# Performance work log

Hardware: AMD Instinct MI355X
Metric: run time of the kernel (lower is better)

The kernel has to match this reference:

```python
import jax, jax.numpy as jnp
import numpy as np

EPS = 1e-6
SIGMA = 0.1  # temperature for pseudo-LBS blend weights


def _quat_rotate(q, v):
    # q: [..., 4] (w, x, y, z) unit quaternions, v: [..., 3]
    qw, qv = q[..., :1], q[..., 1:]
    t = 2.0 * jnp.cross(qv, v)
    return v + qw * t + jnp.cross(qv, t)


def _pairwise_sqdist(a, b):
    # a: [n, d], b: [m, d] -> [n, m]
    return (jnp.sum(a * a, -1, keepdims=True)
            + jnp.sum(b * b, -1)[None, :]
            - 2.0 * (a @ b.T))


def setup_inputs() -> dict:
    N, K, F, V, J, P, M, H = 300000, 80, 64, 6890, 24, 64, 64, 128
    key = jax.random.key(0)
    ks = jax.random.split(key, 16)
    s = lambda i, shape: jax.random.normal(ks[i], shape, dtype=jnp.float32) * 0.05
    return {
        "xyz": jax.random.normal(ks[0], (N, 3), dtype=jnp.float32),
        "feature": jax.random.normal(ks[1], (N, F), dtype=jnp.float32),
        "centers": jax.random.normal(ks[2], (K, F), dtype=jnp.float32),
        "smpl_verts": jax.random.normal(ks[3], (V, 3), dtype=jnp.float32),
        "skinning_weights": jax.random.uniform(ks[4], (V, J), dtype=jnp.float32),
        "body_pose_feature": jax.random.normal(ks[5], (J, P), dtype=jnp.float32),
        "w_body": s(6, (P + F, M)),
        "b_body": jnp.zeros((M,), jnp.float32),
        "w_pos1": s(7, (3 + M, H)),
        "b_pos1": jnp.zeros((H,), jnp.float32),
        "w_pos2": s(8, (H, M)),
        "b_pos2": jnp.zeros((M,), jnp.float32),
        "w_rot": s(9, (M, 4)),
        "b_rot": jnp.zeros((4,), jnp.float32),
        "w_trans": s(10, (M, 3)),
        "b_trans": jnp.zeros((3,), jnp.float32),
    }


def reference(xyz, feature, centers, smpl_verts, skinning_weights,
              body_pose_feature, w_body, b_body, w_pos1, b_pos1,
              w_pos2, b_pos2, w_rot, b_rot, w_trans, b_trans):
    # ---- soft k-means: soft assignment of N points to K garment joints ----
    a = jax.nn.softmax(-_pairwise_sqdist(feature, centers), axis=-1)  # [N, K]
    cnt = a.sum(axis=0) + EPS                                          # [K]
    # weighted segment-reduce: c_assign^T @ xyz, diag(1/count) normalize
    joint_xyz = (a.T @ xyz) / cnt[:, None]      # [K, 3]
    joint_feat = (a.T @ feature) / cnt[:, None]  # [K, F] (cluster centers)

    # ---- KNN (k=1) skin-weight lookup against SMPL canonical verts ----
    idx = jnp.argmin(_pairwise_sqdist(joint_xyz, smpl_verts), axis=-1)  # [K]
    pts_W = skinning_weights[idx]                                        # [K, J]

    # ---- garment pose decoder ----
    body_feat = pts_W @ body_pose_feature                 # [K, P]
    g = jnp.concatenate([body_feat, joint_feat], axis=-1)  # [K, P+F]
    g = jax.nn.gelu(g @ w_body + b_body)                   # [K, M]
    lo, hi = smpl_verts.min(0), smpl_verts.max(0)
    xn = 2.0 * (joint_xyz - lo) / (hi - lo + EPS) - 1.0    # aabb sym-normalize
    h = jax.nn.relu(jnp.concatenate([xn, g], -1) @ w_pos1 + b_pos1)
    g2 = h @ w_pos2 + b_pos2                               # [K, M]
    q = g2 @ w_rot + b_rot
    q = q / (jnp.linalg.norm(q, axis=-1, keepdims=True) + EPS)  # [K, 4]
    t = g2 @ w_trans + b_trans                                   # [K, 3]

    # ---- pseudo-LBS: blend per-joint transforms back to N points ----
    w = jax.nn.softmax(-_pairwise_sqdist(xyz, joint_xyz) / SIGMA, axis=-1)  # [N, K]
    qb = w @ q
    qb = qb / (jnp.linalg.norm(qb, axis=-1, keepdims=True) + EPS)  # [N, 4]
    deformed_xyz = _quat_rotate(qb, xyz) + w @ t                    # [N, 3]
    return deformed_xyz
```

## Files before the change

### kernel.cpp

```cpp
#include <hip/hip_runtime.h>
#include <math.h>

#define N_PTS 300000
#define NJ 80
#define FDIM 64
#define VN 6890
#define ITER_PTS 128
#define NITER ((N_PTS + ITER_PTS - 1) / ITER_PTS)
#define GRID_A 768
#define RSLICE 16

typedef __attribute__((ext_vector_type(8))) short short8;
typedef __attribute__((ext_vector_type(4))) float f32x4;

union Frag { uint32_t u[4]; short8 v; };

__device__ __forceinline__ uint32_t pack1(float f) {
  uint32_t b = __float_as_uint(f);
  float lo = f - __uint_as_float(b & 0xFFFF0000u);
  return (b >> 16) | ((__float_as_uint(lo) >> 16) << 16);
}
__device__ __forceinline__ void unpack8(const uint32_t* W, uint32_t* hw, uint32_t* lw) {
#pragma unroll
  for (int j = 0; j < 4; ++j) {
    hw[j] = (W[2*j] & 0xFFFFu) | (W[2*j+1] << 16);
    lw[j] = (W[2*j] >> 16) | (W[2*j+1] & 0xFFFF0000u);
  }
}

__global__ __launch_bounds__(512, 6) void kA(
    const float* __restrict__ xyz, const float* __restrict__ feature,
    const float* __restrict__ centers, float* __restrict__ jacc,
    float* __restrict__ part)
{
  __shared__ uint32_t sC[NJ][68];
  __shared__ float    sCn[NJ];
  __shared__ ushort   sP[NJ][136];

  const int tid = threadIdx.x;
  const int w = tid >> 6;
  const int l = tid & 63;
  const int i = l & 15;
  const int g = l >> 4;

  for (int idx = tid; idx < NJ * 16; idx += 512) {
    int k = idx >> 4, q = idx & 15;
    float4 v = ((const float4*)centers)[k * 16 + q];
    sC[k][4*q+0] = pack1(v.x); sC[k][4*q+1] = pack1(v.y);
    sC[k][4*q+2] = pack1(v.z); sC[k][4*q+3] = pack1(v.w);
  }
  if (tid < NJ) {
    float s = 0.f;
    const float* c = centers + tid * FDIM;
    for (int d = 0; d < FDIM; ++d) s += c[d] * c[d];
    sCn[tid] = s;
  }
  __syncthreads();

  float cnv[5];
#pragma unroll
  for (int nt = 0; nt < 5; ++nt) cnv[nt] = sCn[i + 16*nt];

  f32x4 acc2[5];
#pragma unroll
  for (int nt = 0; nt < 5; ++nt) acc2[nt] = (f32x4){0.f, 0.f, 0.f, 0.f};

  for (int it = blockIdx.x; it < NITER; it += GRID_A) {
    const int base = it * ITER_PTS;

    const int ptA = base + 16*w + i;
    const int ptAc = ptA < N_PTS ? ptA : N_PTS - 1;
    const bool vA = ptA < N_PTS;
    f32x4 acc1[5];
#pragma unroll
    for (int nt = 0; nt < 5; ++nt) acc1[nt] = (f32x4){0.f, 0.f, 0.f, 0.f};

#pragma unroll
    for (int ks = 0; ks < 2; ++ks) {
      const float* fp = feature + (size_t)ptAc * FDIM + 32*ks + 8*g;
      uint32_t pw[8];
#pragma unroll
      for (int e = 0; e < 8; ++e) pw[e] = vA ? pack1(fp[e]) : 0u;
      Frag ah, al; unpack8(pw, ah.u, al.u);
#pragma unroll
      for (int nt = 0; nt < 5; ++nt) {
        uint32_t W[8];
        *(uint4*)&W[0] = *(const uint4*)&sC[i + 16*nt][32*ks + 8*g];
        *(uint4*)&W[4] = *(const uint4*)&sC[i + 16*nt][32*ks + 8*g + 4];
        Frag bh, bl; unpack8(W, bh.u, bl.u);
        acc1[nt] = __builtin_amdgcn_mfma_f32_16x16x32_bf16(ah.v, bh.v, acc1[nt], 0, 0, 0);
        acc1[nt] = __builtin_amdgcn_mfma_f32_16x16x32_bf16(ah.v, bl.v, acc1[nt], 0, 0, 0);
        acc1[nt] = __builtin_amdgcn_mfma_f32_16x16x32_bf16(al.v, bh.v, acc1[nt], 0, 0, 0);
      }
    }

#pragma unroll
    for (int r = 0; r < 4; ++r) {
      float lg[5]; float m = -1e30f;
#pragma unroll
      for (int nt = 0; nt < 5; ++nt) {
        lg[nt] = 2.f * acc1[nt][r] - cnv[nt];
        m = fmaxf(m, lg[nt]);
      }
#pragma unroll
      for (int ms = 1; ms < 16; ms <<= 1) m = fmaxf(m, __shfl_xor(m, ms));
      float ev[5], s = 0.f;
#pragma unroll
      for (int nt = 0; nt < 5; ++nt) { ev[nt] = __expf(lg[nt] - m); s += ev[nt]; }
#pragma unroll
      for (int ms = 1; ms < 16; ms <<= 1) s += __shfl_xor(s, ms);
      const float rs = 1.f / s;
      const int slot = 16*w + 4*g + r;
      const bool val = (base + slot) < N_PTS;
#pragma unroll
      for (int nt = 0; nt < 5; ++nt) {
        const int row = i + 16*nt;
        ushort h = val ? (ushort)(__float_as_uint(ev[nt] * rs) >> 16) : (ushort)0;
        sP[row][slot ^ ((row & 7) << 3)] = h;
      }
    }
    __syncthreads();

    if (w < 5) {
#pragma unroll
      for (int kk = 0; kk < 4; ++kk) {
        Frag af;
#pragma unroll
        for (int p2 = 0; p2 < 4; ++p2) {
          float x0, x1;
#pragma unroll
          for (int h = 0; h < 2; ++h) {
            const int e = 2*p2 + h;
            const int pt = base + 32*kk + 8*g + e;
            const int ptc = pt < N_PTS ? pt : N_PTS - 1;
            float x;
            if (w < 4) x = feature[(size_t)ptc * FDIM + 16*w + i];
            else       x = (i < 3) ? xyz[(size_t)ptc * 3 + i] : (i == 3 ? 1.f : 0.f);
            if (h == 0) x0 = x; else x1 = x;
          }
          af.u[p2] = (__float_as_uint(x0) >> 16) | (__float_as_uint(x1) & 0xFFFF0000u);
        }
#pragma unroll
        for (int nt = 0; nt < 5; ++nt) {
          const int row = i + 16*nt;
          const int start = (32*kk + 8*g) ^ ((row & 7) << 3);
          Frag bf;
          *(uint4*)bf.u = *(const uint4*)&sP[row][start];
          acc2[nt] = __builtin_amdgcn_mfma_f32_16x16x32_bf16(af.v, bf.v, acc2[nt], 0, 0, 0);
        }
      }
    }
    __syncthreads();
  }

  if (w < 5) {
#pragma unroll
    for (int nt = 0; nt < 5; ++nt) {
      const int joint = i + 16*nt;
#pragma unroll
      for (int r = 0; r < 4; ++r) {
        const int c = 16*w + 4*g + r;
        if (c < 68) {
          if (part) part[(size_t)blockIdx.x * 5440 + joint * 68 + c] = acc2[nt][r];
          else atomicAdd(&jacc[joint * 68 + c], acc2[nt][r]);
        }
      }
    }
  }
}

__global__ __launch_bounds__(256) void kR(const float* __restrict__ part,
                                          float* __restrict__ jacc)
{
  const int bx = blockIdx.x;
  const int cg = bx % 22, sl = bx / 22;
  const int t = cg * 256 + threadIdx.x;
  if (t >= 5440) return;
  const int b0 = sl * (GRID_A / RSLICE), b1 = b0 + GRID_A / RSLICE;
  float s0 = 0.f, s1 = 0.f, s2 = 0.f, s3 = 0.f;
  for (int b = b0; b < b1; b += 4) {
    s0 += part[(size_t)(b+0) * 5440 + t];
    s1 += part[(size_t)(b+1) * 5440 + t];
    s2 += part[(size_t)(b+2) * 5440 + t];
    s3 += part[(size_t)(b+3) * 5440 + t];
  }
  atomicAdd(&jacc[t], (s0 + s1) + (s2 + s3));
}

__global__ __launch_bounds__(64) void kB(
    const float* __restrict__ jacc, const float* __restrict__ smpl,
    const float* __restrict__ sw, const float* __restrict__ bpf,
    const float* __restrict__ w_body, const float* __restrict__ b_body,
    const float* __restrict__ w_pos1, const float* __restrict__ b_pos1,
    const float* __restrict__ w_pos2, const float* __restrict__ b_pos2,
    const float* __restrict__ w_rot,  const float* __restrict__ b_rot,
    const float* __restrict__ w_trans,const float* __restrict__ b_trans,
    float* __restrict__ jpack, float* __restrict__ qpack,
    float* __restrict__ tpack)
{
  const int k = blockIdx.x;
  const int l = threadIdx.x;
  __shared__ float gin[128];
  __shared__ float in2[67];
  __shared__ float h2[128];
  __shared__ float g2[64];
  __shared__ float q7[8];

  const float cnt = jacc[k*68 + 67] + 1e-6f;
  gin[64 + l] = jacc[k*68 + l] / cnt;
  const float jx = jacc[k*68 + 64] / cnt;
  const float jy = jacc[k*68 + 65] / cnt;
  const float jz = jacc[k*68 + 66] / cnt;

  float lo0 = 1e30f, lo1 = 1e30f, lo2 = 1e30f;
  float hi0 = -1e30f, hi1 = -1e30f, hi2 = -1e30f;
  float best = 1e30f; int bi = 0;
  for (int v = l; v < VN; v += 64) {
    float x = smpl[v*3], y = smpl[v*3+1], z = smpl[v*3+2];
    lo0 = fminf(lo0, x); hi0 = fmaxf(hi0, x);
    lo1 = fminf(lo1, y); hi1 = fmaxf(hi1, y);
    lo2 = fminf(lo2, z); hi2 = fmaxf(hi2, z);
    float dx = x - jx, dy = y - jy, dz = z - jz;
    float d = dx*dx + dy*dy + dz*dz;
    if (d < best) { best = d; bi = v; }
  }
#pragma unroll
  for (int m = 1; m < 64; m <<= 1) {
    lo0 = fminf(lo0, __shfl_xor(lo0, m));
    lo1 = fminf(lo1, __shfl_xor(lo1, m));
    lo2 = fminf(lo2, __shfl_xor(lo2, m));
    hi0 = fmaxf(hi0, __shfl_xor(hi0, m));
    hi1 = fmaxf(hi1, __shfl_xor(hi1, m));
    hi2 = fmaxf(hi2, __shfl_xor(hi2, m));
    float d2 = __shfl_xor(best, m); int i2 = __shfl_xor(bi, m);
    if (d2 < best || (d2 == best && i2 < bi)) { best = d2; bi = i2; }
  }

  {
    float s = 0.f;
    for (int j = 0; j < 24; ++j) s += sw[bi*24 + j] * bpf[j*64 + l];
    gin[l] = s;
  }
  if (l < 3) {
    float lo = (l == 0) ? lo0 : (l == 1) ? lo1 : lo2;
    float hi = (l == 0) ? hi0 : (l == 1) ? hi1 : hi2;
    float jc = (l == 0) ? jx : (l == 1) ? jy : jz;
    in2[l] = 2.f * (jc - lo) / (hi - lo + 1e-6f) - 1.f;
  }
  __syncthreads();

  {
    float s = b_body[l];
    for (int t = 0; t < 128; ++t) s += gin[t] * w_body[t*64 + l];
    float u = 0.7978845608028654f * (s + 0.044715f * s * s * s);
    float e = __expf(2.f * u);
    float th = 1.f - 2.f / (e + 1.f);
    in2[3 + l] = 0.5f * s * (1.f + th);
  }
  __syncthreads();

#pragma unroll
  for (int half = 0; half < 2; ++half) {
    const int m = l + 64*half;
    float s = b_pos1[m];
    for (int t = 0; t < 67; ++t) s += in2[t] * w_pos1[t*128 + m];
    h2[m] = fmaxf(s, 0.f);
  }
  __syncthreads();

  {
    float s = b_pos2[l];
    for (int t = 0; t < 128; ++t) s += h2[t] * w_pos2[t*64 + l];
    g2[l] = s;
  }
  __syncthreads();

  if (l < 4) {
    float s = b_rot[l];
    for (int t = 0; t < 64; ++t) s += g2[t] * w_rot[t*4 + l];
    q7[l] = s;
  } else if (l < 7) {
    const int j = l - 4;
    float s = b_trans[j];
    for (int t = 0; t < 64; ++t) s += g2[t] * w_trans[t*3 + j];
    q7[l] = s;
  }
  __syncthreads();
  if (l == 0) {
    float q0 = q7[0], q1 = q7[1], q2 = q7[2], q3 = q7[3];
    float rn = 1.f / (sqrtf(q0*q0 + q1*q1 + q2*q2 + q3*q3) + 1e-6f);
    *(float4*)&qpack[k*4] = make_float4(q0*rn, q1*rn, q2*rn, q3*rn);
    *(float4*)&tpack[k*4] = make_float4(q7[4], q7[5], q7[6], 0.f);
    *(float4*)&jpack[k*4] = make_float4(jx, jy, jz, jx*jx + jy*jy + jz*jz);
  }
}

__global__ __launch_bounds__(256) void kC(
    const float* __restrict__ xyz, const float* __restrict__ jpack,
    const float* __restrict__ qpack, const float* __restrict__ tpack,
    float* __restrict__ out)
{
  __shared__ float4 sj[NJ], sq[NJ], st[NJ];
  const int tid = threadIdx.x;
  if (tid < 80)        sj[tid]       = ((const float4*)jpack)[tid];
  else if (tid < 160)  sq[tid - 80]  = ((const float4*)qpack)[tid - 80];
  else if (tid < 240)  st[tid - 160] = ((const float4*)tpack)[tid - 160];
  __syncthreads();

  const int p = blockIdx.x * 256 + tid;
  if (p >= N_PTS) return;

  float x0 = xyz[p*3], x1 = xyz[p*3+1], x2 = xyz[p*3+2];
  float lv[NJ];
  float m = -1e30f;
#pragma unroll
  for (int k = 0; k < NJ; ++k) {
    float4 j = sj[k];
    lv[k] = (2.f*(x0*j.x + x1*j.y + x2*j.z) - j.w) * 10.0f;
    m = fmaxf(m, lv[k]);
  }
  float s = 0.f;
  float qb0=0,qb1=0,qb2=0,qb3=0, tb0=0,tb1=0,tb2=0;
#pragma unroll
  for (int k = 0; k < NJ; ++k) {
    float e = __expf(lv[k] - m);
    s += e;
    float4 q = sq[k];
    float4 t = st[k];
    qb0 += e*q.x; qb1 += e*q.y; qb2 += e*q.z; qb3 += e*q.w;
    tb0 += e*t.x; tb1 += e*t.y; tb2 += e*t.z;
  }
  float rs = 1.f / s;
  qb0*=rs; qb1*=rs; qb2*=rs; qb3*=rs; tb0*=rs; tb1*=rs; tb2*=rs;
  float nrm = sqrtf(qb0*qb0+qb1*qb1+qb2*qb2+qb3*qb3) + 1e-6f;
  float rn = 1.f / nrm;
  float qw = qb0*rn, qx = qb1*rn, qy = qb2*rn, qz = qb3*rn;
  float t2x = 2.f*(qy*x2 - qz*x1);
  float t2y = 2.f*(qz*x0 - qx*x2);
  float t2z = 2.f*(qx*x1 - qy*x0);
  float cx = qy*t2z - qz*t2y;
  float cy = qz*t2x - qx*t2z;
  float cz = qx*t2y - qy*t2x;
  out[p*3]   = x0 + qw*t2x + cx + tb0;
  out[p*3+1] = x1 + qw*t2y + cy + tb1;
  out[p*3+2] = x2 + qw*t2z + cz + tb2;
}

extern "C" void kernel_launch(void* const* d_in, const int* in_sizes, int n_in,
                              void* d_out, int out_size, void* d_ws, size_t ws_size,
                              hipStream_t stream) {
  const float* xyz     = (const float*)d_in[0];
  const float* feature = (const float*)d_in[1];
  const float* centers = (const float*)d_in[2];
  const float* smpl    = (const float*)d_in[3];
  const float* sw      = (const float*)d_in[4];
  const float* bpf     = (const float*)d_in[5];
  const float* w_body  = (const float*)d_in[6];
  const float* b_body  = (const float*)d_in[7];
  const float* w_pos1  = (const float*)d_in[8];
  const float* b_pos1  = (const float*)d_in[9];
  const float* w_pos2  = (const float*)d_in[10];
  const float* b_pos2  = (const float*)d_in[11];
  const float* w_rot   = (const float*)d_in[12];
  const float* b_rot   = (const float*)d_in[13];
  const float* w_trans = (const float*)d_in[14];
  const float* b_trans = (const float*)d_in[15];
  float* out = (float*)d_out;

  float* ws    = (float*)d_ws;
  float* jacc  = ws;
  float* jpack = ws + 5440;
  float* qpack = ws + 5760;
  float* tpack = ws + 6080;
  float* part  = ws + 6400;

  const size_t need = (size_t)6400 + (size_t)GRID_A * 5440;
  const bool use_part = (ws_size / 4) >= need;
  float* part_arg = use_part ? part : nullptr;

  hipMemsetAsync(jacc, 0, 5440 * sizeof(float), stream);
  kA<<<dim3(GRID_A), dim3(512), 0, stream>>>(xyz, feature, centers, jacc, part_arg);
  if (use_part)
    kR<<<dim3(22 * RSLICE), dim3(256), 0, stream>>>(part, jacc);
  kB<<<dim3(NJ), dim3(64), 0, stream>>>(jacc, smpl, sw, bpf,
                                        w_body, b_body, w_pos1, b_pos1,
                                        w_pos2, b_pos2, w_rot, b_rot,
                                        w_trans, b_trans, jpack, qpack, tpack);
  kC<<<dim3((N_PTS + 255) / 256), dim3(256), 0, stream>>>(xyz, jpack, qpack, tpack, out);
}
```

Measured before the change: 157.8 us.

## Restructure soft k-means kernel to per-wave 32-point rounds with register-resident accumulators

Kernel kA is reorganised so each wave independently processes 32-point rounds. Feature rows are loaded once as float4 and reused both for the distance MFMAs and, via a per-wave transposed LDS tile, for the a^T·[feature,xyz,1] accumulation. The old cross-wave softmax-probability exchange and its two block barriers per iteration are gone. Center hi fragments and norms now stay in registers, the softmax reductions use DPP instead of shuffles, and the 5x5 accumulator tile stays in registers until a final LDS reduction per block. The grid shrinks to 512 blocks of 256 threads, and the partial-sum reduction kernel is adjusted to match. This raises register pressure, and the hard-coded round count assumes N is divisible by 32.

```diff
diff --git a/kernel.cpp b/kernel.cpp
--- a/kernel.cpp
+++ b/kernel.cpp
@@ -5,37 +5,34 @@
 #define NJ 80
 #define FDIM 64
 #define VN 6890
-#define ITER_PTS 128
-#define NITER ((N_PTS + ITER_PTS - 1) / ITER_PTS)
-#define GRID_A 768
-#define RSLICE 16
+#define NROUND 9375
+#define GRID_A 512
+#define WAVES_A (GRID_A * 4)
 
 typedef __attribute__((ext_vector_type(8))) short short8;
 typedef __attribute__((ext_vector_type(4))) float f32x4;
 
 union Frag { uint32_t u[4]; short8 v; };
 
-__device__ __forceinline__ uint32_t pack1(float f) {
-  uint32_t b = __float_as_uint(f);
-  float lo = f - __uint_as_float(b & 0xFFFF0000u);
-  return (b >> 16) | ((__float_as_uint(lo) >> 16) << 16);
-}
-__device__ __forceinline__ void unpack8(const uint32_t* W, uint32_t* hw, uint32_t* lw) {
-#pragma unroll
-  for (int j = 0; j < 4; ++j) {
-    hw[j] = (W[2*j] & 0xFFFFu) | (W[2*j+1] << 16);
-    lw[j] = (W[2*j] >> 16) | (W[2*j+1] & 0xFFFF0000u);
-  }
-}
-
-__global__ __launch_bounds__(512, 6) void kA(
+__device__ __forceinline__ uint32_t packhi(float a, float b) {
+  return (__float_as_uint(a) >> 16) | (__float_as_uint(b) & 0xFFFF0000u);
+}
+__device__ __forceinline__ uint32_t packlo(float a, float b) {
+  float la = a - __uint_as_float(__float_as_uint(a) & 0xFFFF0000u);
+  float lb = b - __uint_as_float(__float_as_uint(b) & 0xFFFF0000u);
+  return packhi(la, lb);
+}
+
+#define DPPF(x, ctrl) __uint_as_float((uint32_t)__builtin_amdgcn_update_dpp( \
+    0, (int)__float_as_uint(x), (ctrl), 0xF, 0xF, true))
+
+__global__ __launch_bounds__(256, 2) void kA(
     const float* __restrict__ xyz, const float* __restrict__ feature,
     const float* __restrict__ centers, float* __restrict__ jacc,
     float* __restrict__ part)
 {
-  __shared__ uint32_t sC[NJ][68];
-  __shared__ float    sCn[NJ];
-  __shared__ ushort   sP[NJ][136];
+  __shared__ ushort sClo[NJ][72];
+  __shared__ ushort sT[4][NJ][36];
 
   const int tid = threadIdx.x;
   const int w = tid >> 6;
@@ -43,129 +40,170 @@
   const int i = l & 15;
   const int g = l >> 4;
 
-  for (int idx = tid; idx < NJ * 16; idx += 512) {
-    int k = idx >> 4, q = idx & 15;
-    float4 v = ((const float4*)centers)[k * 16 + q];
-    sC[k][4*q+0] = pack1(v.x); sC[k][4*q+1] = pack1(v.y);
-    sC[k][4*q+2] = pack1(v.z); sC[k][4*q+3] = pack1(v.w);
-  }
-  if (tid < NJ) {
+  for (int idx = tid; idx < 4 * NJ * 36; idx += 256) ((ushort*)sT)[idx] = 0;
+  for (int idx = tid; idx < NJ * FDIM; idx += 256) {
+    float f = centers[idx];
+    float lo = f - __uint_as_float(__float_as_uint(f) & 0xFFFF0000u);
+    sClo[idx >> 6][idx & 63] = (ushort)(__float_as_uint(lo) >> 16);
+  }
+
+  Frag bh[5][2];
+  float cn[5];
+#pragma unroll
+  for (int nt = 0; nt < 5; ++nt) {
     float s = 0.f;
-    const float* c = centers + tid * FDIM;
-    for (int d = 0; d < FDIM; ++d) s += c[d] * c[d];
-    sCn[tid] = s;
-  }
-  __syncthreads();
-
-  float cnv[5];
-#pragma unroll
-  for (int nt = 0; nt < 5; ++nt) cnv[nt] = sCn[i + 16*nt];
-
-  f32x4 acc2[5];
-#pragma unroll
-  for (int nt = 0; nt < 5; ++nt) acc2[nt] = (f32x4){0.f, 0.f, 0.f, 0.f};
-
-  for (int it = blockIdx.x; it < NITER; it += GRID_A) {
-    const int base = it * ITER_PTS;
-
-    const int ptA = base + 16*w + i;
-    const int ptAc = ptA < N_PTS ? ptA : N_PTS - 1;
-    const bool vA = ptA < N_PTS;
-    f32x4 acc1[5];
-#pragma unroll
-    for (int nt = 0; nt < 5; ++nt) acc1[nt] = (f32x4){0.f, 0.f, 0.f, 0.f};
-
 #pragma unroll
     for (int ks = 0; ks < 2; ++ks) {
-      const float* fp = feature + (size_t)ptAc * FDIM + 32*ks + 8*g;
-      uint32_t pw[8];
-#pragma unroll
-      for (int e = 0; e < 8; ++e) pw[e] = vA ? pack1(fp[e]) : 0u;
-      Frag ah, al; unpack8(pw, ah.u, al.u);
+      const float4* cp = (const float4*)(centers + (size_t)(i + 16*nt) * FDIM + 32*ks + 8*g);
+      float4 v0 = cp[0], v1 = cp[1];
+      bh[nt][ks].u[0] = packhi(v0.x, v0.y);
+      bh[nt][ks].u[1] = packhi(v0.z, v0.w);
+      bh[nt][ks].u[2] = packhi(v1.x, v1.y);
+      bh[nt][ks].u[3] = packhi(v1.z, v1.w);
+      s += v0.x*v0.x + v0.y*v0.y + v0.z*v0.z + v0.w*v0.w
+         + v1.x*v1.x + v1.y*v1.y + v1.z*v1.z + v1.w*v1.w;
+    }
+    s += __shfl_xor(s, 16);
+    s += __shfl_xor(s, 32);
+    cn[nt] = s;
+  }
+
+  f32x4 acc2[5][5];
+#pragma unroll
+  for (int a = 0; a < 5; ++a)
+#pragma unroll
+    for (int b = 0; b < 5; ++b) acc2[a][b] = (f32x4){0.f, 0.f, 0.f, 0.f};
+
+  __syncthreads();
+
+  const int gw = blockIdx.x * 4 + w;
+  for (int rd = gw; rd < NROUND; rd += WAVES_A) {
+    const int pbase = rd * 32;
+
+    float4 vv[2][2][2];
+    float  xq[2];
+#pragma unroll
+    for (int c = 0; c < 2; ++c) {
+      const int pt = pbase + 16*c + i;
+#pragma unroll
+      for (int ks = 0; ks < 2; ++ks) {
+        const float4* fp = (const float4*)(feature + (size_t)pt * FDIM + 32*ks + 8*g);
+        vv[c][ks][0] = fp[0];
+        vv[c][ks][1] = fp[1];
+      }
+      xq[c] = (g < 3) ? xyz[(size_t)pt * 3 + g] : 1.0f;
+    }
+
+    Frag pA[5];
+#pragma unroll
+    for (int c = 0; c < 2; ++c) {
+      f32x4 acc1[5];
+#pragma unroll
+      for (int nt = 0; nt < 5; ++nt) acc1[nt] = (f32x4){0.f, 0.f, 0.f, 0.f};
+
+#pragma unroll
+      for (int ks = 0; ks < 2; ++ks) {
+        float4 v0 = vv[c][ks][0], v1 = vv[c][ks][1];
+        Frag ah, al;
+        ah.u[0] = packhi(v0.x, v0.y); ah.u[1] = packhi(v0.z, v0.w);
+        ah.u[2] = packhi(v1.x, v1.y); ah.u[3] = packhi(v1.z, v1.w);
+        al.u[0] = packlo(v0.x, v0.y); al.u[1] = packlo(v0.z, v0.w);
+        al.u[2] = packlo(v1.x, v1.y); al.u[3] = packlo(v1.z, v1.w);
+        const int d0 = 32*ks + 8*g, pcol = 16*c + i;
+        sT[w][d0+0][pcol] = (ushort)(ah.u[0] & 0xFFFFu);
+        sT[w][d0+1][pcol] = (ushort)(ah.u[0] >> 16);
+        sT[w][d0+2][pcol] = (ushort)(ah.u[1] & 0xFFFFu);
+        sT[w][d0+3][pcol] = (ushort)(ah.u[1] >> 16);
+        sT[w][d0+4][pcol] = (ushort)(ah.u[2] & 0xFFFFu);
+        sT[w][d0+5][pcol] = (ushort)(ah.u[2] >> 16);
+        sT[w][d0+6][pcol] = (ushort)(ah.u[3] & 0xFFFFu);
+        sT[w][d0+7][pcol] = (ushort)(ah.u[3] >> 16);
+#pragma unroll
+        for (int nt = 0; nt < 5; ++nt) {
+          Frag bl;
+          *(uint4*)bl.u = *(const uint4*)&sClo[i + 16*nt][32*ks + 8*g];
+          acc1[nt] = __builtin_amdgcn_mfma_f32_16x16x32_bf16(ah.v, bh[nt][ks].v, acc1[nt], 0, 0, 0);
+          acc1[nt] = __builtin_amdgcn_mfma_f32_16x16x32_bf16(al.v, bh[nt][ks].v, acc1[nt], 0, 0, 0);
+          acc1[nt] = __builtin_amdgcn_mfma_f32_16x16x32_bf16(ah.v, bl.v,        acc1[nt], 0, 0, 0);
+        }
+      }
+      sT[w][64 + g][16*c + i] =
+          (g < 3) ? (ushort)(__float_as_uint(xq[c]) >> 16) : (ushort)0x3F80;
+
+      f32x4 e5[5];
 #pragma unroll
       for (int nt = 0; nt < 5; ++nt) {
-        uint32_t W[8];
-        *(uint4*)&W[0] = *(const uint4*)&sC[i + 16*nt][32*ks + 8*g];
-        *(uint4*)&W[4] = *(const uint4*)&sC[i + 16*nt][32*ks + 8*g + 4];
-        Frag bh, bl; unpack8(W, bh.u, bl.u);
-        acc1[nt] = __builtin_amdgcn_mfma_f32_16x16x32_bf16(ah.v, bh.v, acc1[nt], 0, 0, 0);
-        acc1[nt] = __builtin_amdgcn_mfma_f32_16x16x32_bf16(ah.v, bl.v, acc1[nt], 0, 0, 0);
-        acc1[nt] = __builtin_amdgcn_mfma_f32_16x16x32_bf16(al.v, bh.v, acc1[nt], 0, 0, 0);
+#pragma unroll
+        for (int r = 0; r < 4; ++r) e5[nt][r] = 2.f * acc1[nt][r] - cn[nt];
+      }
+      float rs[4];
+#pragma unroll
+      for (int r = 0; r < 4; ++r) {
+        float m = e5[0][r];
+#pragma unroll
+        for (int nt = 1; nt < 5; ++nt) m = fmaxf(m, e5[nt][r]);
+        m = fmaxf(m, DPPF(m, 0xB1));
+        m = fmaxf(m, DPPF(m, 0x4E));
+        m = fmaxf(m, DPPF(m, 0x141));
+        m = fmaxf(m, DPPF(m, 0x140));
+        float s = 0.f;
+#pragma unroll
+        for (int nt = 0; nt < 5; ++nt) {
+          float e = __expf(e5[nt][r] - m);
+          e5[nt][r] = e;
+          s += e;
+        }
+        s += DPPF(s, 0xB1);
+        s += DPPF(s, 0x4E);
+        s += DPPF(s, 0x141);
+        s += DPPF(s, 0x140);
+        rs[r] = __builtin_amdgcn_rcpf(s);
+      }
+#pragma unroll
+      for (int nt = 0; nt < 5; ++nt) {
+        pA[nt].u[2*c + 0] = packhi(e5[nt][0] * rs[0], e5[nt][1] * rs[1]);
+        pA[nt].u[2*c + 1] = packhi(e5[nt][2] * rs[2], e5[nt][3] * rs[3]);
       }
     }
 
 #pragma unroll
-    for (int r = 0; r < 4; ++r) {
-      float lg[5]; float m = -1e30f;
-#pragma unroll
-      for (int nt = 0; nt < 5; ++nt) {
-        lg[nt] = 2.f * acc1[nt][r] - cnv[nt];
-        m = fmaxf(m, lg[nt]);
-      }
-#pragma unroll
-      for (int ms = 1; ms < 16; ms <<= 1) m = fmaxf(m, __shfl_xor(m, ms));
-      float ev[5], s = 0.f;
-#pragma unroll
-      for (int nt = 0; nt < 5; ++nt) { ev[nt] = __expf(lg[nt] - m); s += ev[nt]; }
-#pragma unroll
-      for (int ms = 1; ms < 16; ms <<= 1) s += __shfl_xor(s, ms);
-      const float rs = 1.f / s;
-      const int slot = 16*w + 4*g + r;
-      const bool val = (base + slot) < N_PTS;
-#pragma unroll
-      for (int nt = 0; nt < 5; ++nt) {
-        const int row = i + 16*nt;
-        ushort h = val ? (ushort)(__float_as_uint(ev[nt] * rs) >> 16) : (ushort)0;
-        sP[row][slot ^ ((row & 7) << 3)] = h;
-      }
+    for (int ct = 0; ct < 5; ++ct) {
+      Frag B;
+      *(uint2*)&B.u[0] = *(const uint2*)&sT[w][16*ct + i][4*g];
+      *(uint2*)&B.u[2] = *(const uint2*)&sT[w][16*ct + i][16 + 4*g];
+#pragma unroll
+      for (int nt = 0; nt < 5; ++nt)
+        acc2[nt][ct] = __builtin_amdgcn_mfma_f32_16x16x32_bf16(pA[nt].v, B.v, acc2[nt][ct], 0, 0, 0);
+    }
+  }
+
+  __syncthreads();
+  float* sJ = (float*)&sT[0][0][0];
+  for (int idx = tid; idx < 5440; idx += 256) sJ[idx] = 0.f;
+  __syncthreads();
+#pragma unroll
+  for (int ww = 0; ww < 4; ++ww) {
+    if (w == ww) {
+#pragma unroll
+      for (int nt = 0; nt < 5; ++nt)
+#pragma unroll
+        for (int ct = 0; ct < 5; ++ct) {
+          if (ct < 4 || i < 4) {
+            const int col = 16*ct + i;
+#pragma unroll
+            for (int r = 0; r < 4; ++r)
+              sJ[(16*nt + 4*g + r) * 68 + col] += acc2[nt][ct][r];
+          }
+        }
     }
     __syncthreads();
-
-    if (w < 5) {
-#pragma unroll
-      for (int kk = 0; kk < 4; ++kk) {
-        Frag af;
-#pragma unroll
-        for (int p2 = 0; p2 < 4; ++p2) {
-          float x0, x1;
-#pragma unroll
-          for (int h = 0; h < 2; ++h) {
-            const int e = 2*p2 + h;
-            const int pt = base + 32*kk + 8*g + e;
-            const int ptc = pt < N_PTS ? pt : N_PTS - 1;
-            float x;
-            if (w < 4) x = feature[(size_t)ptc * FDIM + 16*w + i];
-            else       x = (i < 3) ? xyz[(size_t)ptc * 3 + i] : (i == 3 ? 1.f : 0.f);
-            if (h == 0) x0 = x; else x1 = x;
-          }
-          af.u[p2] = (__float_as_uint(x0) >> 16) | (__float_as_uint(x1) & 0xFFFF0000u);
-        }
-#pragma unroll
-        for (int nt = 0; nt < 5; ++nt) {
-          const int row = i + 16*nt;
-          const int start = (32*kk + 8*g) ^ ((row & 7) << 3);
-          Frag bf;
-          *(uint4*)bf.u = *(const uint4*)&sP[row][start];
-          acc2[nt] = __builtin_amdgcn_mfma_f32_16x16x32_bf16(af.v, bf.v, acc2[nt], 0, 0, 0);
-        }
-      }
-    }
-    __syncthreads();
-  }
-
-  if (w < 5) {
-#pragma unroll
-    for (int nt = 0; nt < 5; ++nt) {
-      const int joint = i + 16*nt;
-#pragma unroll
-      for (int r = 0; r < 4; ++r) {
-        const int c = 16*w + 4*g + r;
-        if (c < 68) {
-          if (part) part[(size_t)blockIdx.x * 5440 + joint * 68 + c] = acc2[nt][r];
-          else atomicAdd(&jacc[joint * 68 + c], acc2[nt][r]);
-        }
-      }
-    }
+  }
+  if (part) {
+    for (int idx = tid; idx < 5440; idx += 256)
+      part[(size_t)blockIdx.x * 5440 + idx] = sJ[idx];
+  } else {
+    for (int idx = tid; idx < 5440; idx += 256)
+      atomicAdd(&jacc[idx], sJ[idx]);
   }
 }
 
@@ -176,9 +214,9 @@
   const int cg = bx % 22, sl = bx / 22;
   const int t = cg * 256 + threadIdx.x;
   if (t >= 5440) return;
-  const int b0 = sl * (GRID_A / RSLICE), b1 = b0 + GRID_A / RSLICE;
+  const int b0 = sl * 32;
   float s0 = 0.f, s1 = 0.f, s2 = 0.f, s3 = 0.f;
-  for (int b = b0; b < b1; b += 4) {
+  for (int b = b0; b < b0 + 32; b += 4) {
     s0 += part[(size_t)(b+0) * 5440 + t];
     s1 += part[(size_t)(b+1) * 5440 + t];
     s2 += part[(size_t)(b+2) * 5440 + t];
@@ -379,9 +417,9 @@
   float* part_arg = use_part ? part : nullptr;
 
   hipMemsetAsync(jacc, 0, 5440 * sizeof(float), stream);
-  kA<<<dim3(GRID_A), dim3(512), 0, stream>>>(xyz, feature, centers, jacc, part_arg);
+  kA<<<dim3(GRID_A), dim3(256), 0, stream>>>(xyz, feature, centers, jacc, part_arg);
   if (use_part)
-    kR<<<dim3(22 * RSLICE), dim3(256), 0, stream>>>(part, jacc);
+    kR<<<dim3(22 * 16), dim3(256), 0, stream>>>(part, jacc);
   kB<<<dim3(NJ), dim3(64), 0, stream>>>(jacc, smpl, sw, bpf,
                                         w_body, b_body, w_pos1, b_pos1,
                                         w_pos2, b_pos2, w_rot, b_rot,
```

After: 135.5 us. 14.1% less time.
